# Optimization experiments

Measured on AMD Instinct MI355X. Metric: run time of the kernel, lower is better.

The kernel has to match this reference:

```python
import jax, jax.numpy as jnp
import numpy as np

TF_ALPHA = 0.125  # teacher-forcing blend used in forward()


def setup_inputs() -> dict:
    key = jax.random.key(0)
    ks = jax.random.split(key, 6)
    B, T, dx, dz, dy = 512, 1024, 32, 64, 256
    return {
        "X": jax.random.normal(ks[0], (B, T, dx), dtype=jnp.float32),
        "A": (jax.random.normal(ks[1], (dz,), dtype=jnp.float32) * 0.1),
        "W1": jax.random.normal(ks[2], (dz, dy), dtype=jnp.float32) / np.sqrt(dy).astype(np.float32),
        "W2": jax.random.normal(ks[3], (dy, dz), dtype=jnp.float32) / np.sqrt(dz).astype(np.float32),
        "h1": jax.random.normal(ks[4], (dz,), dtype=jnp.float32) * 0.01,
        "h2": jax.random.normal(ks[5], (dy,), dtype=jnp.float32) * 0.01,
    }


def reference(X, A, W1, W2, h1, h2):
    # X: (batch, time, dim_x); shallow-PLRNN, dim_x_proj=0, no mean centering, no inputs.
    B, T, dx = X.shape
    dz = A.shape[0]

    def teacher_force(z, f, alpha):
        # blend forcing signal into first dx latent dims where f is not NaN
        blend = alpha * f + (1.0 - alpha) * z[:, :dx]
        return z.at[:, :dx].set(jnp.where(jnp.isnan(f), z[:, :dx], blend))

    # z0 = teacher_force(zeros, X[:,0], alpha=1)
    z0 = teacher_force(jnp.zeros((B, dz), X.dtype), X[:, 0], 1.0)

    Xt = jnp.transpose(X, (1, 0, 2))  # (T, B, dx)

    def step(z, x_t):
        zf = teacher_force(z, x_t, TF_ALPHA)
        # shallow-PLRNN: z' = A*z + W1 @ relu(W2 @ z + h2) + h1
        hidden = jax.nn.relu(jnp.einsum('yz,bz->by', W2, zf) + h2)
        z_new = A * zf + jnp.einsum('zy,by->bz', W1, hidden) + h1
        return z_new, z_new

    _, Z = jax.lax.scan(step, z0, Xt)          # (T, B, dz)
    Z = jnp.transpose(Z, (1, 0, 2))            # (B, T, dz)
    return Z[:, :, :dx]                        # output = first dim_x latent dims
```

## Files before the change

### kernel.cpp

```cpp
#include <hip/hip_runtime.h>

#define BB 512
#define TT 1024
#define DX 32
#define DZ 64
#define DY 256
#define ALPHA 0.125f
#define HP 36

template<int CTRL>
__device__ __forceinline__ float dpp_add(float x) {
    int p = __builtin_amdgcn_update_dpp(0, __float_as_int(x), CTRL, 0xF, 0xF, true);
    return x + __int_as_float(p);
}

__global__ __launch_bounds__(512, 4)
void plrnn_scan(const float* __restrict__ X, const float* __restrict__ A,
                const float* __restrict__ W1, const float* __restrict__ W2,
                const float* __restrict__ h1, const float* __restrict__ h2,
                float* __restrict__ out) {
    const int b   = blockIdx.x;
    const int tid = threadIdx.x;

    const int y    = tid >> 1;
    const int half = tid & 1;
    const int z    = tid >> 3;
    const int oct  = tid & 7;
    const int wv   = tid >> 6;

    __shared__ float zf_s[DZ];
    __shared__ float hid_s[8 * HP];

    float4 w2r[8];
    float4 w1r[8];
#pragma unroll
    for (int j = 0; j < 8; ++j) {
        w2r[j] = *(const float4*)&W2[y * DZ + 32 * half + 4 * j];
        w1r[j] = *(const float4*)&W1[z * DY + 32 * oct + 4 * j];
    }
    const float h2r = h2[y];
    const float Ar  = A[z];
    const float h1r = h1[z];

    const float* Xb = X   + (size_t)b * TT * DX;
    float*       Ob = out + (size_t)b * TT * DX;

    float zfreg = 0.0f;
    if (oct == 0) {
        float zf = 0.0f;
        if (z < DX) { float x0 = Xb[z]; zf = (x0 == x0) ? x0 : 0.0f; }
        zfreg = zf;
        zf_s[z] = zf;
    }
    __syncthreads();

    const int hidx = wv * HP + (y & 31);
    const float* w2f = (const float*)w2r;
    const float* w1f = (const float*)w1r;

    for (int t = 0; t < TT; ++t) {
        float xnext = 0.0f;
        if (oct == 0 && z < DX && (t + 1) < TT) xnext = Xb[(t + 1) * DX + z];

        const float4* zp = (const float4*)(zf_s + 32 * half);
        float a0 = 0.f, a1 = 0.f, a2 = 0.f, a3 = 0.f;
#pragma unroll
        for (int j = 0; j < 8; ++j) {
            float4 v = zp[j];
            a0 = fmaf(w2f[4 * j + 0], v.x, a0);
            a1 = fmaf(w2f[4 * j + 1], v.y, a1);
            a2 = fmaf(w2f[4 * j + 2], v.z, a2);
            a3 = fmaf(w2f[4 * j + 3], v.w, a3);
        }
        float d1 = (a0 + a1) + (a2 + a3);
        d1 = dpp_add<0xB1>(d1);
        if (half == 0) hid_s[hidx] = fmaxf(d1 + h2r, 0.0f);
        __syncthreads();

        const float4* hp = (const float4*)(hid_s + HP * oct);
        float p0 = 0.f, p1 = 0.f, p2 = 0.f, p3 = 0.f;
#pragma unroll
        for (int j = 0; j < 8; ++j) {
            float4 v = hp[j];
            p0 = fmaf(w1f[4 * j + 0], v.x, p0);
            p1 = fmaf(w1f[4 * j + 1], v.y, p1);
            p2 = fmaf(w1f[4 * j + 2], v.z, p2);
            p3 = fmaf(w1f[4 * j + 3], v.w, p3);
        }
        float d2 = (p0 + p1) + (p2 + p3);
        d2 = dpp_add<0xB1>(d2);
        d2 = dpp_add<0x4E>(d2);
        d2 = dpp_add<0x141>(d2);
        if (oct == 0) {
            float znew = fmaf(Ar, zfreg, d2 + h1r);
            float zf = znew;
            if (z < DX) {
                Ob[t * DX + z] = znew;
                zf = (xnext == xnext) ? fmaf(ALPHA, xnext, (1.0f - ALPHA) * znew)
                                      : znew;
            }
            zfreg = zf;
            zf_s[z] = zf;
        }
        __syncthreads();
    }
}

extern "C" void kernel_launch(void* const* d_in, const int* in_sizes, int n_in,
                              void* d_out, int out_size, void* d_ws, size_t ws_size,
                              hipStream_t stream) {
    const float* X  = (const float*)d_in[0];
    const float* A  = (const float*)d_in[1];
    const float* W1 = (const float*)d_in[2];
    const float* W2 = (const float*)d_in[3];
    const float* h1 = (const float*)d_in[4];
    const float* h2 = (const float*)d_in[5];
    float* out = (float*)d_out;

    plrnn_scan<<<BB, 512, 0, stream>>>(X, A, W1, W2, h1, h2, out);
}
```

Measured before the change: 820.7 us.

## Process two batch sequences per block to amortize barriers and latency

Each block now runs two independent batch recurrences at once, sharing the register-resident W1/W2 weights and the per-step barriers. The two sequences interleave their FMA chains, which adds instruction-level parallelism inside each serial time step, and the grid is halved. The cost is twice the per-thread arithmetic per step, higher register pressure (launch bounds lowered to 2 blocks per CU), and fewer blocks, which may leave CUs underfilled with only 256 blocks.

Measured after the change: 1.075 ms. 31.0% more time.

```diff
diff --git a/kernel.cpp b/kernel.cpp
--- a/kernel.cpp
+++ b/kernel.cpp
@@ -14,12 +14,12 @@
     return x + __int_as_float(p);
 }
 
-__global__ __launch_bounds__(512, 4)
+__global__ __launch_bounds__(512, 2)
 void plrnn_scan(const float* __restrict__ X, const float* __restrict__ A,
                 const float* __restrict__ W1, const float* __restrict__ W2,
                 const float* __restrict__ h1, const float* __restrict__ h2,
                 float* __restrict__ out) {
-    const int b   = blockIdx.x;
+    const int bb  = blockIdx.x * 2;
     const int tid = threadIdx.x;
 
     const int y    = tid >> 1;
@@ -28,8 +28,8 @@
     const int oct  = tid & 7;
     const int wv   = tid >> 6;
 
-    __shared__ float zf_s[DZ];
-    __shared__ float hid_s[8 * HP];
+    __shared__ float zf_s[2][DZ];
+    __shared__ float hid_s[2][8 * HP];
 
     float4 w2r[8];
     float4 w1r[8];
@@ -41,17 +41,20 @@
     const float h2r = h2[y];
     const float Ar  = A[z];
     const float h1r = h1[z];
+    const bool  zlt = (z < DX);
 
-    const float* Xb = X   + (size_t)b * TT * DX;
-    float*       Ob = out + (size_t)b * TT * DX;
+    const float* Xb0 = X   + (size_t)bb * TT * DX;
+    const float* Xb1 = Xb0 + (size_t)TT * DX;
+    float*       Ob0 = out + (size_t)bb * TT * DX;
+    float*       Ob1 = Ob0 + (size_t)TT * DX;
 
-    float zfreg = 0.0f;
-    if (oct == 0) {
-        float zf = 0.0f;
-        if (z < DX) { float x0 = Xb[z]; zf = (x0 == x0) ? x0 : 0.0f; }
-        zfreg = zf;
-        zf_s[z] = zf;
+    float zf0 = 0.f, zf1 = 0.f;
+    if (zlt) {
+        float xa = Xb0[z], xb = Xb1[z];
+        zf0 = (xa == xa) ? xa : 0.f;
+        zf1 = (xb == xb) ? xb : 0.f;
     }
+    if (oct == 0) { zf_s[0][z] = zf0; zf_s[1][z] = zf1; }
     __syncthreads();
 
     const int hidx = wv * HP + (y & 31);
@@ -59,49 +62,79 @@
     const float* w1f = (const float*)w1r;
 
     for (int t = 0; t < TT; ++t) {
-        float xnext = 0.0f;
-        if (oct == 0 && z < DX && (t + 1) < TT) xnext = Xb[(t + 1) * DX + z];
+        float xn0 = 0.f, xn1 = 0.f;
+        if (zlt && (t + 1) < TT) {
+            xn0 = Xb0[(t + 1) * DX + z];
+            xn1 = Xb1[(t + 1) * DX + z];
+        }
 
-        const float4* zp = (const float4*)(zf_s + 32 * half);
+        const float4* zp0 = (const float4*)(&zf_s[0][32 * half]);
+        const float4* zp1 = (const float4*)(&zf_s[1][32 * half]);
         float a0 = 0.f, a1 = 0.f, a2 = 0.f, a3 = 0.f;
+        float c0 = 0.f, c1 = 0.f, c2 = 0.f, c3 = 0.f;
 #pragma unroll
         for (int j = 0; j < 8; ++j) {
-            float4 v = zp[j];
-            a0 = fmaf(w2f[4 * j + 0], v.x, a0);
-            a1 = fmaf(w2f[4 * j + 1], v.y, a1);
-            a2 = fmaf(w2f[4 * j + 2], v.z, a2);
-            a3 = fmaf(w2f[4 * j + 3], v.w, a3);
+            float4 va = zp0[j];
+            float4 vb = zp1[j];
+            a0 = fmaf(w2f[4 * j + 0], va.x, a0);
+            a1 = fmaf(w2f[4 * j + 1], va.y, a1);
+            a2 = fmaf(w2f[4 * j + 2], va.z, a2);
+            a3 = fmaf(w2f[4 * j + 3], va.w, a3);
+            c0 = fmaf(w2f[4 * j + 0], vb.x, c0);
+            c1 = fmaf(w2f[4 * j + 1], vb.y, c1);
+            c2 = fmaf(w2f[4 * j + 2], vb.z, c2);
+            c3 = fmaf(w2f[4 * j + 3], vb.w, c3);
         }
-        float d1 = (a0 + a1) + (a2 + a3);
-        d1 = dpp_add<0xB1>(d1);
-        if (half == 0) hid_s[hidx] = fmaxf(d1 + h2r, 0.0f);
+        float d1a = (a0 + a1) + (a2 + a3);
+        float d1b = (c0 + c1) + (c2 + c3);
+        d1a = dpp_add<0xB1>(d1a);
+        d1b = dpp_add<0xB1>(d1b);
+        if (half == 0) {
+            hid_s[0][hidx] = fmaxf(d1a + h2r, 0.0f);
+            hid_s[1][hidx] = fmaxf(d1b + h2r, 0.0f);
+        }
         __syncthreads();
 
-        const float4* hp = (const float4*)(hid_s + HP * oct);
+        const float4* hp0 = (const float4*)(&hid_s[0][HP * oct]);
+        const float4* hp1 = (const float4*)(&hid_s[1][HP * oct]);
         float p0 = 0.f, p1 = 0.f, p2 = 0.f, p3 = 0.f;
+        float q0 = 0.f, q1 = 0.f, q2 = 0.f, q3 = 0.f;
 #pragma unroll
         for (int j = 0; j < 8; ++j) {
-            float4 v = hp[j];
-            p0 = fmaf(w1f[4 * j + 0], v.x, p0);
-            p1 = fmaf(w1f[4 * j + 1], v.y, p1);
-            p2 = fmaf(w1f[4 * j + 2], v.z, p2);
-            p3 = fmaf(w1f[4 * j + 3], v.w, p3);
+            float4 va = hp0[j];
+            float4 vb = hp1[j];
+            p0 = fmaf(w1f[4 * j + 0], va.x, p0);
+            p1 = fmaf(w1f[4 * j + 1], va.y, p1);
+            p2 = fmaf(w1f[4 * j + 2], va.z, p2);
+            p3 = fmaf(w1f[4 * j + 3], va.w, p3);
+            q0 = fmaf(w1f[4 * j + 0], vb.x, q0);
+            q1 = fmaf(w1f[4 * j + 1], vb.y, q1);
+            q2 = fmaf(w1f[4 * j + 2], vb.z, q2);
+            q3 = fmaf(w1f[4 * j + 3], vb.w, q3);
         }
-        float d2 = (p0 + p1) + (p2 + p3);
-        d2 = dpp_add<0xB1>(d2);
-        d2 = dpp_add<0x4E>(d2);
-        d2 = dpp_add<0x141>(d2);
-        if (oct == 0) {
-            float znew = fmaf(Ar, zfreg, d2 + h1r);
-            float zf = znew;
-            if (z < DX) {
-                Ob[t * DX + z] = znew;
-                zf = (xnext == xnext) ? fmaf(ALPHA, xnext, (1.0f - ALPHA) * znew)
-                                      : znew;
+        float d2a = (p0 + p1) + (p2 + p3);
+        float d2b = (q0 + q1) + (q2 + q3);
+        d2a = dpp_add<0xB1>(d2a);
+        d2b = dpp_add<0xB1>(d2b);
+        d2a = dpp_add<0x4E>(d2a);
+        d2b = dpp_add<0x4E>(d2b);
+        d2a = dpp_add<0x141>(d2a);
+        d2b = dpp_add<0x141>(d2b);
+
+        float zn0 = fmaf(Ar, zf0, d2a + h1r);
+        float zn1 = fmaf(Ar, zf1, d2b + h1r);
+        float nz0 = zn0, nz1 = zn1;
+        if (zlt) {
+            if (oct == 0) {
+                Ob0[t * DX + z] = zn0;
+                Ob1[t * DX + z] = zn1;
             }
-            zfreg = zf;
-            zf_s[z] = zf;
+            nz0 = (xn0 == xn0) ? fmaf(ALPHA, xn0, (1.0f - ALPHA) * zn0) : zn0;
+            nz1 = (xn1 == xn1) ? fmaf(ALPHA, xn1, (1.0f - ALPHA) * zn1) : zn1;
         }
+        zf0 = nz0;
+        zf1 = nz1;
+        if (oct == 0) { zf_s[0][z] = zf0; zf_s[1][z] = zf1; }
         __syncthreads();
     }
 }
@@ -117,5 +150,5 @@
     const float* h2 = (const float*)d_in[5];
     float* out = (float*)d_out;
 
-    plrnn_scan<<<BB, 512, 0, stream>>>(X, A, W1, W2, h1, h2, out);
+    plrnn_scan<<<BB / 2, 512, 0, stream>>>(X, A, W1, W2, h1, h2, out);
 }
```
